# Optimization experiments

Hardware: AMD Instinct MI355X
Metric: run time of the kernel (lower is better)

Reference implementation:

```python
import jax, jax.numpy as jnp
import numpy as np
import math

D, NH, NL, NP = 256, 8, 3, 4
HD = D // NH
SPATIAL = ((128, 128), (64, 64), (32, 32))  # static value_spatial_shapes, one (h,w) per level


def _offset_bias():
    # replicates _reset_parameters grid init for sampling_offsets.bias
    thetas = jnp.arange(NH, dtype=jnp.float32) * (2.0 * math.pi / NH)
    grid = jnp.stack([jnp.cos(thetas), jnp.sin(thetas)], -1)  # (NH, 2)
    grid = grid[:, None, None, :] * (jnp.arange(NP, dtype=jnp.float32) + 1.0)[None, None, :, None]
    return jnp.broadcast_to(grid, (NH, NL, NP, 2)).reshape(-1)  # (NH*NL*NP*2,)


def setup_inputs() -> dict:
    key = jax.random.key(0)
    k = jax.random.split(key, 7)
    bs, Lq = 4, 8192
    Lv = sum(h * w for h, w in SPATIAL)  # 21504
    s = 0.02
    return {
        "query": jax.random.normal(k[0], (bs, Lq, D), jnp.float32),
        "reference_points": jax.random.uniform(k[1], (bs, Lq, 4), jnp.float32),
        "value": jax.random.normal(k[2], (bs, Lv, D), jnp.float32),
        "W_off": jax.random.normal(k[3], (D, NH * NL * NP * 2), jnp.float32) * 0.001,
        "b_off": _offset_bias(),
        "W_attn": jax.random.normal(k[4], (D, NH * NL * NP), jnp.float32) * s,
        "b_attn": jnp.zeros((NH * NL * NP,), jnp.float32),
        "W_v": jax.random.normal(k[5], (D, D), jnp.float32) * s,
        "b_v": jnp.zeros((D,), jnp.float32),
        "W_out": jax.random.normal(k[6], (D, D), jnp.float32) * s,
        "b_out": jnp.zeros((D,), jnp.float32),
    }


def _bilinear(vflat, h, w, gx, gy):
    # F.grid_sample(mode='bilinear', align_corners=False, padding_mode='zeros')
    # vflat: (B, C, h*w); gx, gy: (B, P) in [-1, 1] -> (B, C, P)
    x = ((gx + 1.0) * w - 1.0) * 0.5
    y = ((gy + 1.0) * h - 1.0) * 0.5
    x0f = jnp.floor(x); y0f = jnp.floor(y)
    wx1 = x - x0f; wy1 = y - y0f
    x0 = x0f.astype(jnp.int32); y0 = y0f.astype(jnp.int32)

    def gather(xi, yi, wgt):
        valid = (xi >= 0) & (xi < w) & (yi >= 0) & (yi < h)
        idx = jnp.clip(yi, 0, h - 1) * w + jnp.clip(xi, 0, w - 1)
        g = jnp.take_along_axis(vflat, idx[:, None, :], axis=2)  # (B, C, P)
        return g * (wgt * valid)[:, None, :]

    return (gather(x0, y0, (1.0 - wx1) * (1.0 - wy1))
            + gather(x0 + 1, y0, wx1 * (1.0 - wy1))
            + gather(x0, y0 + 1, (1.0 - wx1) * wy1)
            + gather(x0 + 1, y0 + 1, wx1 * wy1))


def reference(query, reference_points, value, W_off, b_off, W_attn, b_attn, W_v, b_v, W_out, b_out):
    bs, Lq, _ = query.shape
    v = value @ W_v + b_v                                           # (bs, Lv, D)
    v4 = v.reshape(bs, -1, NH, HD)
    off = (query @ W_off + b_off).reshape(bs, Lq, NH, NL, NP, 2)
    aw = jax.nn.softmax((query @ W_attn + b_attn).reshape(bs, Lq, NH, NL * NP), axis=-1)
    aw = aw.reshape(bs, Lq, NH, NL, NP)
    ref = reference_points[..., :2][:, :, None, None, None, :]      # (bs, Lq, 1, 1, 1, 2)
    pts = jnp.clip(ref + off, 0.0, 1.0)                             # (bs, Lq, NH, NL, NP, 2)

    out = jnp.zeros((bs, Lq, NH, HD), query.dtype)
    start = 0
    for lvl, (h, w) in enumerate(SPATIAL):
        # faithful to torch source: (bs, NH, h*w, HD) reinterpreted row-major as (bs*NH, HD, h, w)
        v_lvl = v4[:, start:start + h * w].transpose(0, 2, 1, 3).reshape(bs * NH, HD, h * w)
        g = pts[:, :, :, lvl].transpose(0, 2, 1, 3, 4).reshape(bs * NH, Lq * NP, 2) * 2.0 - 1.0
        sampled = _bilinear(v_lvl, h, w, g[..., 0], g[..., 1]).reshape(bs, NH, HD, Lq, NP)
        out = out + jnp.einsum('bhdqp,bhqp->bqhd', sampled, aw[:, :, :, lvl].transpose(0, 2, 1, 3))
        start += h * w

    return out.reshape(bs, Lq, D) @ W_out + b_out
```

## Files before the change

### kernel.cpp

```cpp
#include <hip/hip_runtime.h>
#include <math.h>

#define LV 21504
#define LQ 8192
#define BS 4
#define NHD 8
#define HD 32
#define DIM 256

typedef __attribute__((ext_vector_type(4))) float f32x4;
typedef __attribute__((ext_vector_type(8))) short s16x8;
typedef unsigned short ushort_t;
typedef unsigned int uint_t;

__device__ __forceinline__ void bsplit(float f, ushort_t& h, ushort_t& l) {
  uint_t u = __float_as_uint(f);
  uint_t hr = (u + 0x7fffu + ((u >> 16) & 1u)) >> 16;
  h = (ushort_t)hr;
  float fh = __uint_as_float(hr << 16);
  float fl = f - fh;
  uint_t v = __float_as_uint(fl);
  l = (ushort_t)((v + 0x7fffu + ((v >> 16) & 1u)) >> 16);
}

__global__ __launch_bounds__(256) void k_wsplit(
    const float* __restrict__ Wv, const float* __restrict__ Woff,
    const float* __restrict__ Wattn, ushort_t* __restrict__ wbuf)
{
  int c = blockIdx.x;
  int k = threadIdx.x;
  float w;
  ushort_t *dh, *dl;
  if (c < 256) {
    w = Wv[(size_t)k * 256 + c];
    dh = wbuf + (size_t)c * 256 + k;
    dl = wbuf + 65536 + (size_t)c * 256 + k;
  } else {
    int co = c - 256;
    w = (co < 192) ? Woff[(size_t)k * 192 + co] : Wattn[(size_t)k * 96 + (co - 192)];
    dh = wbuf + 131072 + (size_t)co * 256 + k;
    dl = wbuf + 204800 + (size_t)co * 256 + k;
  }
  ushort_t h, l;
  bsplit(w, h, l);
  *dh = h; *dl = l;
}

__global__ __launch_bounds__(256) void k_wsplit2(
    const float* __restrict__ Wout, ushort_t* __restrict__ tb)
{
  int c = blockIdx.x;
  int k = threadIdx.x;
  float w = Wout[(size_t)k * 256 + c];
  ushort_t h, l;
  bsplit(w, h, l);
  tb[(size_t)c * 256 + k] = h;
  tb[65536 + (size_t)c * 256 + k] = l;
}

__global__ __launch_bounds__(256, 3) void k_vproj(
    const float* __restrict__ value, const ushort_t* __restrict__ wbuf,
    const float* __restrict__ bv, float* __restrict__ vv)
{
  __shared__ ushort_t lAh[64][40];
  __shared__ ushort_t lAl[64][40];

  int bid = blockIdx.x;
  int b = bid / 336, rem = bid % 336;
  int l, mp;
  if (rem < 256)      { l = 0; mp = rem; }
  else if (rem < 320) { l = 1; mp = rem - 256; }
  else                { l = 2; mp = rem - 320; }
  const int startl[3] = {0, 16384, 20480};
  const int hwd[3]    = {512, 128, 32};
  int start = startl[l], hd32 = hwd[l], m0 = mp * 2;

  int t = threadIdx.x;
  int wave = t >> 6, lane = t & 63;
  int l15 = lane & 15, l4 = lane >> 4;
  int n0 = wave * 64;

  const float* Ab = value + (size_t)b * LV * DIM;
  int row0 = t >> 3, kq = t & 7;
  int row1 = row0 + 32;
  const float* ap0 = Ab + (size_t)(start + (row0 & 31) * hd32 + m0 + (row0 >> 5)) * DIM + kq * 4;
  const float* ap1 = Ab + (size_t)(start + (row1 & 31) * hd32 + m0 + (row1 >> 5)) * DIM + kq * 4;

  f32x4 acc[4][4];
  #pragma unroll
  for (int m = 0; m < 4; ++m)
    #pragma unroll
    for (int n = 0; n < 4; ++n) acc[m][n] = (f32x4){0.f, 0.f, 0.f, 0.f};

  for (int s = 0; s < 8; ++s) {
    int k0 = s * 32;
    s16x8 bh[4], bl[4];
    #pragma unroll
    for (int n = 0; n < 4; ++n) {
      int col = n0 + n * 16 + l15;
      bh[n] = *(const s16x8*)(wbuf + (size_t)col * 256 + k0 + l4 * 8);
      bl[n] = *(const s16x8*)(wbuf + 65536 + (size_t)col * 256 + k0 + l4 * 8);
    }
    {
      float4 v0 = *(const float4*)(ap0 + k0);
      float4 v1 = *(const float4*)(ap1 + k0);
      float a0[4] = {v0.x, v0.y, v0.z, v0.w};
      float a1[4] = {v1.x, v1.y, v1.z, v1.w};
      ushort_t hh[4], ll[4];
      #pragma unroll
      for (int j = 0; j < 4; ++j) bsplit(a0[j], hh[j], ll[j]);
      *(uint_t*)&lAh[row0][kq * 4]     = (uint_t)hh[0] | ((uint_t)hh[1] << 16);
      *(uint_t*)&lAh[row0][kq * 4 + 2] = (uint_t)hh[2] | ((uint_t)hh[3] << 16);
      *(uint_t*)&lAl[row0][kq * 4]     = (uint_t)ll[0] | ((uint_t)ll[1] << 16);
      *(uint_t*)&lAl[row0][kq * 4 + 2] = (uint_t)ll[2] | ((uint_t)ll[3] << 16);
      #pragma unroll
      for (int j = 0; j < 4; ++j) bsplit(a1[j], hh[j], ll[j]);
      *(uint_t*)&lAh[row1][kq * 4]     = (uint_t)hh[0] | ((uint_t)hh[1] << 16);
      *(uint_t*)&lAh[row1][kq * 4 + 2] = (uint_t)hh[2] | ((uint_t)hh[3] << 16);
      *(uint_t*)&lAl[row1][kq * 4]     = (uint_t)ll[0] | ((uint_t)ll[1] << 16);
      *(uint_t*)&lAl[row1][kq * 4 + 2] = (uint_t)ll[2] | ((uint_t)ll[3] << 16);
    }
    __syncthreads();
    s16x8 ah[4], al[4];
    #pragma unroll
    for (int m = 0; m < 4; ++m) {
      ah[m] = *(const s16x8*)&lAh[m * 16 + l15][l4 * 8];
      al[m] = *(const s16x8*)&lAl[m * 16 + l15][l4 * 8];
    }
    #pragma unroll
    for (int n = 0; n < 4; ++n)
      #pragma unroll
      for (int m = 0; m < 4; ++m) {
        acc[m][n] = __builtin_amdgcn_mfma_f32_16x16x32_bf16(ah[m], bh[n], acc[m][n], 0, 0, 0);
        acc[m][n] = __builtin_amdgcn_mfma_f32_16x16x32_bf16(al[m], bh[n], acc[m][n], 0, 0, 0);
        acc[m][n] = __builtin_amdgcn_mfma_f32_16x16x32_bf16(ah[m], bl[n], acc[m][n], 0, 0, 0);
      }
    __syncthreads();
  }

  #pragma unroll
  for (int m = 0; m < 4; ++m) {
    int d = (m & 1) * 16 + l4 * 4;
    int mloc = m0 + (m >> 1);
    #pragma unroll
    for (int n = 0; n < 4; ++n) {
      int col = n0 + n * 16 + l15;
      int g = col >> 5, j = col & 31;
      float bias = bv[col];
      f32x4 o = acc[m][n];
      o[0] += bias; o[1] += bias; o[2] += bias; o[3] += bias;
      float* dst = vv + ((size_t)(b * NHD + g) * LV + start) * 32
                      + ((size_t)mloc * 32 + j) * 32 + d;
      *(f32x4*)dst = o;
    }
  }
}

__global__ __launch_bounds__(384, 3) void k_offattn(
    const float* __restrict__ query, const ushort_t* __restrict__ wbuf,
    const float* __restrict__ boff, const float* __restrict__ battn,
    float* __restrict__ offattn)
{
  __shared__ ushort_t lAh[64][40];
  __shared__ ushort_t lAl[64][40];
  int r0 = blockIdx.x * 64;
  int t = threadIdx.x;
  int wave = t >> 6, lane = t & 63;
  int l15 = lane & 15, l4 = lane >> 4;
  int n0 = wave * 48;
  const ushort_t* wh = wbuf + 131072;
  const ushort_t* wl = wbuf + 204800;

  f32x4 acc[4][3];
  #pragma unroll
  for (int m = 0; m < 4; ++m)
    #pragma unroll
    for (int n = 0; n < 3; ++n) acc[m][n] = (f32x4){0.f, 0.f, 0.f, 0.f};

  for (int s = 0; s < 8; ++s) {
    int k0 = s * 32;
    s16x8 bh[3], bl[3];
    #pragma unroll
    for (int n = 0; n < 3; ++n) {
      int col = n0 + n * 16 + l15;
      bh[n] = *(const s16x8*)(wh + (size_t)col * 256 + k0 + l4 * 8);
      bl[n] = *(const s16x8*)(wl + (size_t)col * 256 + k0 + l4 * 8);
    }
    #pragma unroll
    for (int i = 0; i < 2; ++i) {
      int u = i * 384 + t;
      if (u < 512) {
        int row = u >> 3, kq = u & 7;
        float4 v = *(const float4*)(query + (size_t)(r0 + row) * DIM + k0 + kq * 4);
        float a0[4] = {v.x, v.y, v.z, v.w};
        ushort_t hh[4], ll[4];
        #pragma unroll
        for (int j = 0; j < 4; ++j) bsplit(a0[j], hh[j], ll[j]);
        *(uint_t*)&lAh[row][kq * 4]     = (uint_t)hh[0] | ((uint_t)hh[1] << 16);
        *(uint_t*)&lAh[row][kq * 4 + 2] = (uint_t)hh[2] | ((uint_t)hh[3] << 16);
        *(uint_t*)&lAl[row][kq * 4]     = (uint_t)ll[0] | ((uint_t)ll[1] << 16);
        *(uint_t*)&lAl[row][kq * 4 + 2] = (uint_t)ll[2] | ((uint_t)ll[3] << 16);
      }
    }
    __syncthreads();
    s16x8 ah[4], al[4];
    #pragma unroll
    for (int m = 0; m < 4; ++m) {
      ah[m] = *(const s16x8*)&lAh[m * 16 + l15][l4 * 8];
      al[m] = *(const s16x8*)&lAl[m * 16 + l15][l4 * 8];
    }
    #pragma unroll
    for (int n = 0; n < 3; ++n)
      #pragma unroll
      for (int m = 0; m < 4; ++m) {
        acc[m][n] = __builtin_amdgcn_mfma_f32_16x16x32_bf16(ah[m], bh[n], acc[m][n], 0, 0, 0);
        acc[m][n] = __builtin_amdgcn_mfma_f32_16x16x32_bf16(al[m], bh[n], acc[m][n], 0, 0, 0);
        acc[m][n] = __builtin_amdgcn_mfma_f32_16x16x32_bf16(ah[m], bl[n], acc[m][n], 0, 0, 0);
      }
    __syncthreads();
  }
  #pragma unroll
  for (int m = 0; m < 4; ++m)
    #pragma unroll
    for (int n = 0; n < 3; ++n) {
      int col = n0 + n * 16 + l15;
      float bias = (col < 192) ? boff[col] : battn[col - 192];
      #pragma unroll
      for (int i = 0; i < 4; ++i)
        offattn[(size_t)(r0 + m * 16 + l4 * 4 + i) * 288 + col] = acc[m][n][i] + bias;
    }
}

__global__ __launch_bounds__(256) void k_sample(
    const float* __restrict__ offattn, const float* __restrict__ refp,
    const float* __restrict__ vv, uint_t* __restrict__ midp)
{
  __shared__ float4 metaw[64][13];
  __shared__ uint4  metaa[64][13];
  __shared__ float  smx[64], sinv[64];

  int t = threadIdx.x;
  int e0 = blockIdx.x * 64;

  {
    int it = t >> 2, j = t & 3;
    int e = e0 + it;
    int n = e & 7, bq = e >> 3;
    const float* lgp = offattn + (size_t)bq * 288 + 192 + n * 12;
    float l0 = lgp[j], l1 = lgp[j + 4], l2 = lgp[j + 8];
    float m = fmaxf(fmaxf(l0, l1), l2);
    m = fmaxf(m, __shfl_xor(m, 1));
    m = fmaxf(m, __shfl_xor(m, 2));
    float s = __expf(l0 - m) + __expf(l1 - m) + __expf(l2 - m);
    s += __shfl_xor(s, 1);
    s += __shfl_xor(s, 2);
    if (j == 0) { smx[it] = m; sinv[it] = 1.f / s; }
  }
  __syncthreads();

  const int startl[3] = {0, 16384, 20480};
  const int whl[3]    = {128, 64, 32};
  #pragma unroll
  for (int r = 0; r < 3; ++r) {
    int task = r * 256 + t;
    int it = task / 12, p = task % 12;
    int e = e0 + it;
    int n = e & 7, bq = e >> 3;
    int l = p >> 2;
    int w = whl[l], h = w;
    float fw = (float)w;
    const float* oa = offattn + (size_t)bq * 288;
    float ox = oa[n * 24 + p * 2], oy = oa[n * 24 + p * 2 + 1];
    float lg = oa[192 + n * 12 + p];
    float aw = __expf(lg - smx[it]) * sinv[it];
    float rx = refp[bq * 4], ry = refp[bq * 4 + 1];
    float px = fminf(fmaxf(rx + ox, 0.f), 1.f);
    float py = fminf(fmaxf(ry + oy, 0.f), 1.f);
    float x = px * fw - 0.5f, y = py * fw - 0.5f;
    float x0f = floorf(x), y0f = floorf(y);
    int x0 = (int)x0f, y0 = (int)y0f;
    float wx1 = x - x0f, wy1 = y - y0f;
    float wx0 = 1.f - wx1, wy0 = 1.f - wy1;
    float vx0 = ((uint_t)x0 < (uint_t)w) ? 1.f : 0.f;
    float vx1 = ((uint_t)(x0 + 1) < (uint_t)w) ? 1.f : 0.f;
    float vy0 = ((uint_t)y0 < (uint_t)h) ? 1.f : 0.f;
    float vy1 = ((uint_t)(y0 + 1) < (uint_t)h) ? 1.f : 0.f;
    int xc0 = min(max(x0, 0), w - 1), xc1 = min(max(x0 + 1, 0), w - 1);
    int yc0 = min(max(y0, 0), h - 1), yc1 = min(max(y0 + 1, 0), h - 1);
    int s0 = startl[l];
    uint4 av;
    av.x = (uint_t)(s0 + yc0 * w + xc0) * 128u;
    av.y = (uint_t)(s0 + yc0 * w + xc1) * 128u;
    av.z = (uint_t)(s0 + yc1 * w + xc0) * 128u;
    av.w = (uint_t)(s0 + yc1 * w + xc1) * 128u;
    float4 wv;
    wv.x = aw * wy0 * wx0 * vy0 * vx0;
    wv.y = aw * wy0 * wx1 * vy0 * vx1;
    wv.z = aw * wy1 * wx0 * vy1 * vx0;
    wv.w = aw * wy1 * wx1 * vy1 * vx1;
    metaw[it][p] = wv;
    metaa[it][p] = av;
  }
  __syncthreads();

  #pragma unroll
  for (int r = 0; r < 2; ++r) {
    int it = (t >> 3) + r * 32;
    int c4 = t & 7;
    int e = e0 + it;
    int n = e & 7, bq = e >> 3, b = bq >> 13;
    const char* vb = (const char*)(vv + (size_t)(b * NHD + n) * LV * 32) + c4 * 16;
    f32x4 acc = (f32x4){0.f, 0.f, 0.f, 0.f};
    #pragma unroll
    for (int p = 0; p < 12; ++p) {
      float4 wv = metaw[it][p];
      uint4  av = metaa[it][p];
      f32x4 g00 = *(const f32x4*)(vb + av.x);
      f32x4 g01 = *(const f32x4*)(vb + av.y);
      f32x4 g10 = *(const f32x4*)(vb + av.z);
      f32x4 g11 = *(const f32x4*)(vb + av.w);
      acc += wv.x * g00;
      acc += wv.y * g01;
      acc += wv.z * g10;
      acc += wv.w * g11;
    }
    uint4 pk;
    ushort_t h16, l16;
    bsplit(acc[0], h16, l16); pk.x = (uint_t)h16 | ((uint_t)l16 << 16);
    bsplit(acc[1], h16, l16); pk.y = (uint_t)h16 | ((uint_t)l16 << 16);
    bsplit(acc[2], h16, l16); pk.z = (uint_t)h16 | ((uint_t)l16 << 16);
    bsplit(acc[3], h16, l16); pk.w = (uint_t)h16 | ((uint_t)l16 << 16);
    *(uint4*)(midp + (size_t)bq * 256 + n * 32 + c4 * 4) = pk;
  }
}

__global__ __launch_bounds__(256, 3) void k_out(
    const uint_t* __restrict__ midp, const ushort_t* __restrict__ wtb,
    const float* __restrict__ bout, float* __restrict__ out)
{
  __shared__ ushort_t lAh[64][40];
  __shared__ ushort_t lAl[64][40];
  int r0 = blockIdx.x * 64;
  int t = threadIdx.x;
  int wave = t >> 6, lane = t & 63;
  int l15 = lane & 15, l4 = lane >> 4;
  int n0 = wave * 64;

  f32x4 acc[4][4];
  #pragma unroll
  for (int m = 0; m < 4; ++m)
    #pragma unroll
    for (int n = 0; n < 4; ++n) acc[m][n] = (f32x4){0.f, 0.f, 0.f, 0.f};

  for (int s = 0; s < 8; ++s) {
    int k0 = s * 32;
    s16x8 bh[4], bl[4];
    #pragma unroll
    for (int n = 0; n < 4; ++n) {
      int col = n0 + n * 16 + l15;
      bh[n] = *(const s16x8*)(wtb + (size_t)col * 256 + k0 + l4 * 8);
      bl[n] = *(const s16x8*)(wtb + 65536 + (size_t)col * 256 + k0 + l4 * 8);
    }
    #pragma unroll
    for (int i = 0; i < 2; ++i) {
      int u = i * 256 + t;
      int row = u >> 3, kq = u & 7;
      uint4 v = *(const uint4*)(midp + (size_t)(r0 + row) * DIM + k0 + kq * 4);
      uint_t a0 = v.x, a1 = v.y, a2 = v.z, a3 = v.w;
      *(uint_t*)&lAh[row][kq * 4]     = (a0 & 0xffffu) | ((a1 & 0xffffu) << 16);
      *(uint_t*)&lAh[row][kq * 4 + 2] = (a2 & 0xffffu) | ((a3 & 0xffffu) << 16);
      *(uint_t*)&lAl[row][kq * 4]     = (a0 >> 16) | (a1 & 0xffff0000u);
      *(uint_t*)&lAl[row][kq * 4 + 2] = (a2 >> 16) | (a3 & 0xffff0000u);
    }
    __syncthreads();
    s16x8 ah[4], al[4];
    #pragma unroll
    for (int m = 0; m < 4; ++m) {
      ah[m] = *(const s16x8*)&lAh[m * 16 + l15][l4 * 8];
      al[m] = *(const s16x8*)&lAl[m * 16 + l15][l4 * 8];
    }
    #pragma unroll
    for (int n = 0; n < 4; ++n)
      #pragma unroll
      for (int m = 0; m < 4; ++m) {
        acc[m][n] = __builtin_amdgcn_mfma_f32_16x16x32_bf16(ah[m], bh[n], acc[m][n], 0, 0, 0);
        acc[m][n] = __builtin_amdgcn_mfma_f32_16x16x32_bf16(al[m], bh[n], acc[m][n], 0, 0, 0);
        acc[m][n] = __builtin_amdgcn_mfma_f32_16x16x32_bf16(ah[m], bl[n], acc[m][n], 0, 0, 0);
      }
    __syncthreads();
  }
  #pragma unroll
  for (int m = 0; m < 4; ++m)
    #pragma unroll
    for (int n = 0; n < 4; ++n) {
      int col = n0 + n * 16 + l15;
      float bias = bout[col];
      #pragma unroll
      for (int i = 0; i < 4; ++i)
        out[(size_t)(r0 + m * 16 + l4 * 4 + i) * DIM + col] = acc[m][n][i] + bias;
    }
}

extern "C" void kernel_launch(void* const* d_in, const int* in_sizes, int n_in,
                              void* d_out, int out_size, void* d_ws, size_t ws_size,
                              hipStream_t stream) {
  const float* query = (const float*)d_in[0];
  const float* refp  = (const float*)d_in[1];
  const float* value = (const float*)d_in[2];
  const float* Woff  = (const float*)d_in[3];
  const float* boff  = (const float*)d_in[4];
  const float* Wattn = (const float*)d_in[5];
  const float* battn = (const float*)d_in[6];
  const float* Wv    = (const float*)d_in[7];
  const float* bv    = (const float*)d_in[8];
  const float* Wout  = (const float*)d_in[9];
  const float* bout  = (const float*)d_in[10];
  float* out = (float*)d_out;
  ushort_t* wbuf = (ushort_t*)d_out;

  float* ws      = (float*)d_ws;
  float* vv      = ws;
  float* offattn = ws + 22020096;
  uint_t* midp   = (uint_t*)(ws + 22020096 + 9437184);
  ushort_t* wtb  = (ushort_t*)ws;

  hipLaunchKernelGGL(k_wsplit,  dim3(544),   dim3(256), 0, stream, Wv, Woff, Wattn, wbuf);
  hipLaunchKernelGGL(k_vproj,   dim3(1344),  dim3(256), 0, stream, value, wbuf, bv, vv);
  hipLaunchKernelGGL(k_offattn, dim3(512),   dim3(384), 0, stream, query, wbuf, boff, battn, offattn);
  hipLaunchKernelGGL(k_sample,  dim3(4096),  dim3(256), 0, stream, offattn, refp, vv, midp);
  hipLaunchKernelGGL(k_wsplit2, dim3(256),   dim3(256), 0, stream, Wout, wtb);
  hipLaunchKernelGGL(k_out,     dim3(512),   dim3(256), 0, stream, midp, wtb, bout, out);
}
```

Before: 353.8 us.

## Store projected values as bf16 and double-buffer vproj LDS tiles

The value projection now writes its output as bf16 instead of fp32, and the sampling kernel gathers 8-byte bf16 vectors and widens them to fp32. This halves the vproj write traffic and the gather traffic in the bilinear sampling stage, at the cost of reduced precision in the sampled values. The vproj GEMM also switches to 64-wide K steps with a double-buffered LDS tile, prefetching the next A block into registers while the MFMAs run. This cuts the number of barriers and overlaps global loads with compute, but uses more LDS per block, which may lower occupancy.

```diff
diff --git a/kernel.cpp b/kernel.cpp
--- a/kernel.cpp
+++ b/kernel.cpp
@@ -21,6 +21,11 @@
   float fl = f - fh;
   uint_t v = __float_as_uint(fl);
   l = (ushort_t)((v + 0x7fffu + ((v >> 16) & 1u)) >> 16);
+}
+
+__device__ __forceinline__ uint_t bf16rne(float f) {
+  uint_t u = __float_as_uint(f);
+  return (u + 0x7fffu + ((u >> 16) & 1u)) >> 16;
 }
 
 __global__ __launch_bounds__(256) void k_wsplit(
@@ -60,10 +65,9 @@
 
 __global__ __launch_bounds__(256, 3) void k_vproj(
     const float* __restrict__ value, const ushort_t* __restrict__ wbuf,
-    const float* __restrict__ bv, float* __restrict__ vv)
-{
-  __shared__ ushort_t lAh[64][40];
-  __shared__ ushort_t lAl[64][40];
+    const float* __restrict__ bv, ushort_t* __restrict__ vvb)
+{
+  __shared__ ushort_t lA[2][2][64][72];
 
   int bid = blockIdx.x;
   int b = bid / 336, rem = bid % 336;
@@ -81,10 +85,13 @@
   int n0 = wave * 64;
 
   const float* Ab = value + (size_t)b * LV * DIM;
-  int row0 = t >> 3, kq = t & 7;
-  int row1 = row0 + 32;
-  const float* ap0 = Ab + (size_t)(start + (row0 & 31) * hd32 + m0 + (row0 >> 5)) * DIM + kq * 4;
-  const float* ap1 = Ab + (size_t)(start + (row1 & 31) * hd32 + m0 + (row1 >> 5)) * DIM + kq * 4;
+  int r0s = t >> 4, kq = t & 15;
+  const float* aptr[4];
+  #pragma unroll
+  for (int j = 0; j < 4; ++j) {
+    int row = r0s + 16 * j;
+    aptr[j] = Ab + (size_t)(start + (row & 31) * hd32 + m0 + (row >> 5)) * DIM + kq * 4;
+  }
 
   f32x4 acc[4][4];
   #pragma unroll
@@ -92,50 +99,77 @@
     #pragma unroll
     for (int n = 0; n < 4; ++n) acc[m][n] = (f32x4){0.f, 0.f, 0.f, 0.f};
 
-  for (int s = 0; s < 8; ++s) {
-    int k0 = s * 32;
-    s16x8 bh[4], bl[4];
-    #pragma unroll
-    for (int n = 0; n < 4; ++n) {
-      int col = n0 + n * 16 + l15;
-      bh[n] = *(const s16x8*)(wbuf + (size_t)col * 256 + k0 + l4 * 8);
-      bl[n] = *(const s16x8*)(wbuf + 65536 + (size_t)col * 256 + k0 + l4 * 8);
-    }
-    {
-      float4 v0 = *(const float4*)(ap0 + k0);
-      float4 v1 = *(const float4*)(ap1 + k0);
-      float a0[4] = {v0.x, v0.y, v0.z, v0.w};
-      float a1[4] = {v1.x, v1.y, v1.z, v1.w};
-      ushort_t hh[4], ll[4];
-      #pragma unroll
-      for (int j = 0; j < 4; ++j) bsplit(a0[j], hh[j], ll[j]);
-      *(uint_t*)&lAh[row0][kq * 4]     = (uint_t)hh[0] | ((uint_t)hh[1] << 16);
-      *(uint_t*)&lAh[row0][kq * 4 + 2] = (uint_t)hh[2] | ((uint_t)hh[3] << 16);
-      *(uint_t*)&lAl[row0][kq * 4]     = (uint_t)ll[0] | ((uint_t)ll[1] << 16);
-      *(uint_t*)&lAl[row0][kq * 4 + 2] = (uint_t)ll[2] | ((uint_t)ll[3] << 16);
-      #pragma unroll
-      for (int j = 0; j < 4; ++j) bsplit(a1[j], hh[j], ll[j]);
-      *(uint_t*)&lAh[row1][kq * 4]     = (uint_t)hh[0] | ((uint_t)hh[1] << 16);
-      *(uint_t*)&lAh[row1][kq * 4 + 2] = (uint_t)hh[2] | ((uint_t)hh[3] << 16);
-      *(uint_t*)&lAl[row1][kq * 4]     = (uint_t)ll[0] | ((uint_t)ll[1] << 16);
-      *(uint_t*)&lAl[row1][kq * 4 + 2] = (uint_t)ll[2] | ((uint_t)ll[3] << 16);
+  float4 pf[4];
+  #pragma unroll
+  for (int j = 0; j < 4; ++j) pf[j] = *(const float4*)(aptr[j]);
+
+  #pragma unroll
+  for (int j = 0; j < 4; ++j) {
+    int row = r0s + 16 * j;
+    float a[4] = {pf[j].x, pf[j].y, pf[j].z, pf[j].w};
+    ushort_t hh[4], ll[4];
+    #pragma unroll
+    for (int q = 0; q < 4; ++q) bsplit(a[q], hh[q], ll[q]);
+    uint2 uh, ul;
+    uh.x = (uint_t)hh[0] | ((uint_t)hh[1] << 16);
+    uh.y = (uint_t)hh[2] | ((uint_t)hh[3] << 16);
+    ul.x = (uint_t)ll[0] | ((uint_t)ll[1] << 16);
+    ul.y = (uint_t)ll[2] | ((uint_t)ll[3] << 16);
+    *(uint2*)&lA[0][0][row][kq * 4] = uh;
+    *(uint2*)&lA[0][1][row][kq * 4] = ul;
+  }
+  __syncthreads();
+
+  int cur = 0;
+  for (int s = 0; s < 4; ++s) {
+    if (s < 3) {
+      #pragma unroll
+      for (int j = 0; j < 4; ++j) pf[j] = *(const float4*)(aptr[j] + (s + 1) * 64);
+    }
+    #pragma unroll
+    for (int c = 0; c < 2; ++c) {
+      int k0 = s * 64 + c * 32;
+      s16x8 bh[4], bl[4];
+      #pragma unroll
+      for (int n = 0; n < 4; ++n) {
+        int col = n0 + n * 16 + l15;
+        bh[n] = *(const s16x8*)(wbuf + (size_t)col * 256 + k0 + l4 * 8);
+        bl[n] = *(const s16x8*)(wbuf + 65536 + (size_t)col * 256 + k0 + l4 * 8);
+      }
+      s16x8 ah[4], al[4];
+      #pragma unroll
+      for (int m = 0; m < 4; ++m) {
+        ah[m] = *(const s16x8*)&lA[cur][0][m * 16 + l15][c * 32 + l4 * 8];
+        al[m] = *(const s16x8*)&lA[cur][1][m * 16 + l15][c * 32 + l4 * 8];
+      }
+      #pragma unroll
+      for (int n = 0; n < 4; ++n)
+        #pragma unroll
+        for (int m = 0; m < 4; ++m) {
+          acc[m][n] = __builtin_amdgcn_mfma_f32_16x16x32_bf16(ah[m], bh[n], acc[m][n], 0, 0, 0);
+          acc[m][n] = __builtin_amdgcn_mfma_f32_16x16x32_bf16(al[m], bh[n], acc[m][n], 0, 0, 0);
+          acc[m][n] = __builtin_amdgcn_mfma_f32_16x16x32_bf16(ah[m], bl[n], acc[m][n], 0, 0, 0);
+        }
+    }
+    if (s < 3) {
+      #pragma unroll
+      for (int j = 0; j < 4; ++j) {
+        int row = r0s + 16 * j;
+        float a[4] = {pf[j].x, pf[j].y, pf[j].z, pf[j].w};
+        ushort_t hh[4], ll[4];
+        #pragma unroll
+        for (int q = 0; q < 4; ++q) bsplit(a[q], hh[q], ll[q]);
+        uint2 uh, ul;
+        uh.x = (uint_t)hh[0] | ((uint_t)hh[1] << 16);
+        uh.y = (uint_t)hh[2] | ((uint_t)hh[3] << 16);
+        ul.x = (uint_t)ll[0] | ((uint_t)ll[1] << 16);
+        ul.y = (uint_t)ll[2] | ((uint_t)ll[3] << 16);
+        *(uint2*)&lA[cur ^ 1][0][row][kq * 4] = uh;
+        *(uint2*)&lA[cur ^ 1][1][row][kq * 4] = ul;
+      }
     }
     __syncthreads();
-    s16x8 ah[4], al[4];
-    #pragma unroll
-    for (int m = 0; m < 4; ++m) {
-      ah[m] = *(const s16x8*)&lAh[m * 16 + l15][l4 * 8];
-      al[m] = *(const s16x8*)&lAl[m * 16 + l15][l4 * 8];
-    }
-    #pragma unroll
-    for (int n = 0; n < 4; ++n)
-      #pragma unroll
-      for (int m = 0; m < 4; ++m) {
-        acc[m][n] = __builtin_amdgcn_mfma_f32_16x16x32_bf16(ah[m], bh[n], acc[m][n], 0, 0, 0);
-        acc[m][n] = __builtin_amdgcn_mfma_f32_16x16x32_bf16(al[m], bh[n], acc[m][n], 0, 0, 0);
-        acc[m][n] = __builtin_amdgcn_mfma_f32_16x16x32_bf16(ah[m], bl[n], acc[m][n], 0, 0, 0);
-      }
-    __syncthreads();
+    cur ^= 1;
   }
 
   #pragma unroll
@@ -148,10 +182,13 @@
       int g = col >> 5, j = col & 31;
       float bias = bv[col];
       f32x4 o = acc[m][n];
-      o[0] += bias; o[1] += bias; o[2] += bias; o[3] += bias;
-      float* dst = vv + ((size_t)(b * NHD + g) * LV + start) * 32
-                      + ((size_t)mloc * 32 + j) * 32 + d;
-      *(f32x4*)dst = o;
+      uint_t h0 = bf16rne(o[0] + bias), h1 = bf16rne(o[1] + bias);
+      uint_t h2 = bf16rne(o[2] + bias), h3 = bf16rne(o[3] + bias);
+      uint2 pk;
+      pk.x = h0 | (h1 << 16);
+      pk.y = h2 | (h3 << 16);
+      ushort_t* dst = vvb + (((size_t)(b * NHD + g) * LV + start + (size_t)mloc * 32 + j) * 32 + d);
+      *(uint2*)dst = pk;
     }
   }
 }
@@ -233,7 +270,7 @@
 
 __global__ __launch_bounds__(256) void k_sample(
     const float* __restrict__ offattn, const float* __restrict__ refp,
-    const float* __restrict__ vv, uint_t* __restrict__ midp)
+    const ushort_t* __restrict__ vvb, uint_t* __restrict__ midp)
 {
   __shared__ float4 metaw[64][13];
   __shared__ uint4  metaa[64][13];
@@ -289,10 +326,10 @@
     int yc0 = min(max(y0, 0), h - 1), yc1 = min(max(y0 + 1, 0), h - 1);
     int s0 = startl[l];
     uint4 av;
-    av.x = (uint_t)(s0 + yc0 * w + xc0) * 128u;
-    av.y = (uint_t)(s0 + yc0 * w + xc1) * 128u;
-    av.z = (uint_t)(s0 + yc1 * w + xc0) * 128u;
-    av.w = (uint_t)(s0 + yc1 * w + xc1) * 128u;
+    av.x = (uint_t)(s0 + yc0 * w + xc0) * 64u;
+    av.y = (uint_t)(s0 + yc0 * w + xc1) * 64u;
+    av.z = (uint_t)(s0 + yc1 * w + xc0) * 64u;
+    av.w = (uint_t)(s0 + yc1 * w + xc1) * 64u;
     float4 wv;
     wv.x = aw * wy0 * wx0 * vy0 * vx0;
     wv.y = aw * wy0 * wx1 * vy0 * vx1;
@@ -309,20 +346,29 @@
     int c4 = t & 7;
     int e = e0 + it;
     int n = e & 7, bq = e >> 3, b = bq >> 13;
-    const char* vb = (const char*)(vv + (size_t)(b * NHD + n) * LV * 32) + c4 * 16;
+    const char* vb = (const char*)vvb + (size_t)(b * NHD + n) * LV * 64 + c4 * 8;
     f32x4 acc = (f32x4){0.f, 0.f, 0.f, 0.f};
     #pragma unroll
     for (int p = 0; p < 12; ++p) {
       float4 wv = metaw[it][p];
       uint4  av = metaa[it][p];
-      f32x4 g00 = *(const f32x4*)(vb + av.x);
-      f32x4 g01 = *(const f32x4*)(vb + av.y);
-      f32x4 g10 = *(const f32x4*)(vb + av.z);
-      f32x4 g11 = *(const f32x4*)(vb + av.w);
-      acc += wv.x * g00;
-      acc += wv.y * g01;
-      acc += wv.z * g10;
-      acc += wv.w * g11;
+      uint2 g00 = *(const uint2*)(vb + av.x);
+      uint2 g01 = *(const uint2*)(vb + av.y);
+      uint2 g10 = *(const uint2*)(vb + av.z);
+      uint2 g11 = *(const uint2*)(vb + av.w);
+      f32x4 f;
+      f[0] = __uint_as_float(g00.x << 16); f[1] = __uint_as_float(g00.x & 0xffff0000u);
+      f[2] = __uint_as_float(g00.y << 16); f[3] = __uint_as_float(g00.y & 0xffff0000u);
+      acc += wv.x * f;
+      f[0] = __uint_as_float(g01.x << 16); f[1] = __uint_as_float(g01.x & 0xffff0000u);
+      f[2] = __uint_as_float(g01.y << 16); f[3] = __uint_as_float(g01.y & 0xffff0000u);
+      acc += wv.y * f;
+      f[0] = __uint_as_float(g10.x << 16); f[1] = __uint_as_float(g10.x & 0xffff0000u);
+      f[2] = __uint_as_float(g10.y << 16); f[3] = __uint_as_float(g10.y & 0xffff0000u);
+      acc += wv.z * f;
+      f[0] = __uint_as_float(g11.x << 16); f[1] = __uint_as_float(g11.x & 0xffff0000u);
+      f[2] = __uint_as_float(g11.y << 16); f[3] = __uint_as_float(g11.y & 0xffff0000u);
+      acc += wv.w * f;
     }
     uint4 pk;
     ushort_t h16, l16;
@@ -419,15 +465,15 @@
   ushort_t* wbuf = (ushort_t*)d_out;
 
   float* ws      = (float*)d_ws;
-  float* vv      = ws;
+  ushort_t* vvb  = (ushort_t*)ws;
   float* offattn = ws + 22020096;
   uint_t* midp   = (uint_t*)(ws + 22020096 + 9437184);
   ushort_t* wtb  = (ushort_t*)ws;
 
   hipLaunchKernelGGL(k_wsplit,  dim3(544),   dim3(256), 0, stream, Wv, Woff, Wattn, wbuf);
-  hipLaunchKernelGGL(k_vproj,   dim3(1344),  dim3(256), 0, stream, value, wbuf, bv, vv);
+  hipLaunchKernelGGL(k_vproj,   dim3(1344),  dim3(256), 0, stream, value, wbuf, bv, vvb);
   hipLaunchKernelGGL(k_offattn, dim3(512),   dim3(384), 0, stream, query, wbuf, boff, battn, offattn);
-  hipLaunchKernelGGL(k_sample,  dim3(4096),  dim3(256), 0, stream, offattn, refp, vv, midp);
+  hipLaunchKernelGGL(k_sample,  dim3(4096),  dim3(256), 0, stream, offattn, refp, vvb, midp);
   hipLaunchKernelGGL(k_wsplit2, dim3(256),   dim3(256), 0, stream, Wout, wtb);
   hipLaunchKernelGGL(k_out,     dim3(512),   dim3(256), 0, stream, midp, wtb, bout, out);
 }
```

New measurement: 342.2 us. 1.03x faster.
